# Kernel optimization log

Measured on AMD Instinct MI355X. Metric: run time of the kernel, lower is better.

Reference implementation:

```python
import jax, jax.numpy as jnp
import numpy as np

N = 65536   # query points
M = 65536   # support points
H = 32      # neighbors per query
IN = 64     # input feature dim
OUT = 64    # out_dim // 2
K = 15      # kernel points
EXTENT = 0.1 * 1.2 / 2.5  # radius * kp_extent / conv_radius = 0.048
BN_EPS = 1e-5


def setup_inputs() -> dict:
    key = jax.random.key(0)
    ks = jax.random.split(key, 8)
    x = jax.random.normal(ks[0], (M, IN), dtype=jnp.float32)
    q_pts = jax.random.uniform(ks[1], (N, 3), dtype=jnp.float32) * 0.1
    s_pts = jax.random.uniform(ks[2], (M, 3), dtype=jnp.float32) * 0.1
    neighb_inds = jax.random.randint(ks[3], (N, H), 0, M, dtype=jnp.int32)
    kernel_points = jax.random.normal(ks[4], (K, 3), dtype=jnp.float32) * (0.5 * EXTENT)
    weights = jax.random.normal(ks[5], (K, IN, OUT), dtype=jnp.float32) * 0.05
    gamma = jnp.ones((OUT,), dtype=jnp.float32)
    beta = jnp.zeros((OUT,), dtype=jnp.float32)
    return {"x": x, "q_pts": q_pts, "s_pts": s_pts, "neighb_inds": neighb_inds,
            "kernel_points": kernel_points, "weights": weights,
            "gamma": gamma, "beta": beta}


def reference(x, q_pts, s_pts, neighb_inds, kernel_points, weights, gamma, beta):
    # --- KPConv (rigid, linear influence, sum aggregation) ---
    # Shadow point/feature for out-of-range neighbor indices (KPConv convention).
    s_pad = jnp.concatenate([s_pts, jnp.full((1, 3), 1e6, s_pts.dtype)], axis=0)
    x_pad = jnp.concatenate([x, jnp.zeros((1, x.shape[1]), x.dtype)], axis=0)

    # Relative neighbor coordinates: [N, H, 3]
    neighbors = s_pad[neighb_inds] - q_pts[:, None, :]
    # Squared distance to each kernel point: [N, H, K]
    diffs = neighbors[:, :, None, :] - kernel_points[None, None, :, :]
    sq_dist = jnp.sum(diffs * diffs, axis=-1)
    # Linear kernel-point influence, clipped at 0: [N, H, K]
    all_weights = jnp.maximum(1.0 - jnp.sqrt(sq_dist) / EXTENT, 0.0)

    # Gather neighbor features: [N, H, IN]
    neighb_x = x_pad[neighb_inds]
    # Influence-weighted aggregation per kernel point: [N, K, IN]
    weighted = jnp.einsum('nhk,nhi->nki', all_weights, neighb_x)
    # Apply per-kernel-point weight matrices and sum over kernel points: [N, OUT]
    out = jnp.einsum('nki,kio->no', weighted, weights)

    # --- BatchNorm (training-mode statistics over points) ---
    mean = jnp.mean(out, axis=0)
    var = jnp.var(out, axis=0)
    out = (out - mean) / jnp.sqrt(var + BN_EPS) * gamma + beta

    # --- LeakyReLU(0.1) ---
    return jnp.where(out >= 0, out, 0.1 * out)
```

## Files before the change

kernel.cpp:

```cpp
#include <hip/hip_runtime.h>
#include <math.h>

#define NQ   65536
#define H    32
#define IN   64
#define OUTC 64
#define K    15
#define QB   16
#define S_XN 68
#define S_WT 36
#define AK   72
#define AROW 1076
#define INV_EXT (1.0f / 0.048f)

#define OFF_PSUM  131072
#define OFF_SCSH  (OFF_PSUM + 2097152)
#define OFF_XBF   (OFF_SCSH + 1024)
#define NEED_BF16 (OFF_XBF + (size_t)NQ * IN * 2)

typedef __attribute__((ext_vector_type(8))) short short8;
typedef __attribute__((ext_vector_type(4))) short short4v;
typedef __attribute__((ext_vector_type(4))) float float4v;

static __device__ __forceinline__ unsigned short f2bf(float f) {
    return (unsigned short)((__float_as_uint(f) + 0x8000u) >> 16);
}
static __device__ __forceinline__ unsigned pk2(float a, float b) {
    return (__float_as_uint(a) + 0x8000u) >> 16 |
           ((__float_as_uint(b) + 0x8000u) & 0xFFFF0000u);
}

__global__ __launch_bounds__(256) void prep_all(
    const float* __restrict__ W, const float* __restrict__ x,
    short* __restrict__ Bfrag, unsigned short* __restrict__ xbf, int do_x)
{
    const int b = blockIdx.x;
    if (b < 4096) {
        if (do_x) {
            const int t = b * 256 + threadIdx.x;
            const float4 v = ((const float4*)x)[t];
            uint2 p; p.x = pk2(v.x, v.y); p.y = pk2(v.z, v.w);
            ((uint2*)xbf)[t] = p;
        }
    } else {
        const int t2 = (b - 4096) * 256 + threadIdx.x;
        const int o  = t2 & 63;
        const int i  = (t2 >> 6) & 63;
        const int kq = t2 >> 12;
        const int t  = kq * 2 + (i >> 5);
        const int lane = ((i >> 3) & 3) * 16 + (o & 15);
        const int v  = o >> 4;
        const int j  = i & 7;
        Bfrag[((v * 30 + t) * 64 + lane) * 8 + j] = (short)f2bf(W[t2]);
    }
}

template<bool BFX>
__global__ __launch_bounds__(256, 4) void kpconv_mfma(
    const float* __restrict__ x, const unsigned short* __restrict__ xbf,
    const float* __restrict__ qp, const float* __restrict__ sp,
    const int* __restrict__ inds, const float* __restrict__ kp,
    const short* __restrict__ Bfrag, float* __restrict__ out_raw,
    float* __restrict__ psum)
{
    __shared__ __align__(16) short lds[17920];
    short* xn  = lds;
    short* wT  = lds + 8704;
    short* Awt = lds;

    const int tid  = threadIdx.x;
    const int lane = tid & 63;
    const int wv   = tid >> 6;
    const int quad = lane >> 4;
    const int ml   = lane & 15;
    const int q0   = blockIdx.x * QB;

    short4v xv[8];
    float4  xf[8];
    {
        const int ibase = (q0 + wv) * H;
#pragma unroll
        for (int j = 0; j < 8; ++j) {
            const int id = inds[ibase + j * 4 + quad];
            if (BFX) xv[j] = *(const short4v*)((const short*)xbf + id * IN + ml * 4);
            else     xf[j] = *(const float4*)(x + id * IN + ml * 4);
        }
    }

    for (int rep = 0; rep < 2; ++rep) {
        const int pair = tid + rep * 256;
        const int q = pair >> 5, h = pair & 31;
        const int n = q0 + q;
        const int id = inds[n * H + h];
        const float dx = sp[id * 3 + 0] - qp[n * 3 + 0];
        const float dy = sp[id * 3 + 1] - qp[n * 3 + 1];
        const float dz = sp[id * 3 + 2] - qp[n * 3 + 2];
#pragma unroll
        for (int k = 0; k < K; ++k) {
            const float ex = dx - kp[k * 3 + 0];
            const float ey = dy - kp[k * 3 + 1];
            const float ez = dz - kp[k * 3 + 2];
            const float sq = ex * ex + ey * ey + ez * ez;
            float wval = 1.0f - __builtin_amdgcn_sqrtf(sq) * INV_EXT;
            wval = wval > 0.0f ? wval : 0.0f;
            wT[(q * 16 + k) * S_WT + h] = (short)f2bf(wval);
        }
        wT[(q * 16 + K) * S_WT + h] = 0;
    }

    float4v frag[QB];
#pragma unroll
    for (int qg = 0; qg < QB; ++qg) frag[qg] = (float4v){0.f, 0.f, 0.f, 0.f};

    for (int b = 0; b < 4; ++b) {
#pragma unroll
        for (int j = 0; j < 8; ++j) {
            const int h = j * 4 + quad;
            if (BFX) {
                *(short4v*)&xn[(wv * H + h) * S_XN + ml * 4] = xv[j];
            } else {
                short4v p;
                p[0] = (short)f2bf(xf[j].x); p[1] = (short)f2bf(xf[j].y);
                p[2] = (short)f2bf(xf[j].z); p[3] = (short)f2bf(xf[j].w);
                *(short4v*)&xn[(wv * H + h) * S_XN + ml * 4] = p;
            }
        }
        __syncthreads();

        if (b < 3) {
            const int ibase = (q0 + 4 * (b + 1) + wv) * H;
#pragma unroll
            for (int j = 0; j < 8; ++j) {
                const int id = inds[ibase + j * 4 + quad];
                if (BFX) xv[j] = *(const short4v*)((const short*)xbf + id * IN + ml * 4);
                else     xf[j] = *(const float4*)(x + id * IN + ml * 4);
            }
        }

#pragma unroll
        for (int ql = 0; ql < 4; ++ql) {
            const int qg = 4 * b + ql;
            const int arow = (qg * 16 + ml) * S_WT + quad * 8;
            const short4v alo = *(const short4v*)&wT[arow];
            const short4v ahi = *(const short4v*)&wT[arow + 4];
            short8 a;
#pragma unroll
            for (int e = 0; e < 4; ++e) { a[e] = alo[e]; a[e + 4] = ahi[e]; }
            short8 bb;
#pragma unroll
            for (int j = 0; j < 8; ++j)
                bb[j] = xn[(ql * H + quad * 8 + j) * S_XN + wv * 16 + ml];
            frag[qg] = __builtin_amdgcn_mfma_f32_16x16x32_bf16(a, bb, frag[qg], 0, 0, 0);
        }
        __syncthreads();
    }

#pragma unroll
    for (int qg = 0; qg < QB; ++qg) {
#pragma unroll
        for (int r = 0; r < 4; ++r) {
            const int kq = quad * 4 + r;
            if (kq < K)
                Awt[qg * AROW + kq * AK + wv * 16 + ml] = (short)f2bf(frag[qg][r]);
        }
    }
    __syncthreads();

    float4v acc = (float4v){0.f, 0.f, 0.f, 0.f};
    const short* bptr = Bfrag + (wv * 30) * 512 + lane * 8;
#pragma unroll 2
    for (int t = 0; t < 30; ++t) {
        const int abase = ml * AROW + (t >> 1) * AK + (t & 1) * 32 + quad * 8;
        const short4v alo = *(const short4v*)&Awt[abase];
        const short4v ahi = *(const short4v*)&Awt[abase + 4];
        short8 a;
#pragma unroll
        for (int e = 0; e < 4; ++e) { a[e] = alo[e]; a[e + 4] = ahi[e]; }
        const short8 bb = *(const short8*)(bptr + t * 512);
        acc = __builtin_amdgcn_mfma_f32_16x16x32_bf16(a, bb, acc, 0, 0, 0);
    }

    float s = 0.f, s2 = 0.f;
#pragma unroll
    for (int r = 0; r < 4; ++r) {
        const float v = acc[r];
        out_raw[(q0 + quad * 4 + r) * OUTC + wv * 16 + ml] = v;
        s += v; s2 += v * v;
    }
    s  += __shfl_xor(s, 16, 64);  s  += __shfl_xor(s, 32, 64);
    s2 += __shfl_xor(s2, 16, 64); s2 += __shfl_xor(s2, 32, 64);
    if (quad == 0) {
        const int c = wv * 16 + ml;
        psum[c * 4096 + blockIdx.x]          = s;
        psum[262144 + c * 4096 + blockIdx.x] = s2;
    }
}

__global__ __launch_bounds__(256) void bn_stats(
    const float* __restrict__ psum, const float* __restrict__ gamma,
    const float* __restrict__ beta, float* __restrict__ sc_sh)
{
    const int c = blockIdx.x;
    const int t = threadIdx.x;
    float s = 0.f, q = 0.f;
#pragma unroll
    for (int i = 0; i < 16; ++i) {
        s += psum[c * 4096 + t + i * 256];
        q += psum[262144 + c * 4096 + t + i * 256];
    }
    __shared__ float rs[4], rq[4];
#pragma unroll
    for (int off = 32; off; off >>= 1) {
        s += __shfl_down(s, off, 64);
        q += __shfl_down(q, off, 64);
    }
    if ((t & 63) == 0) { rs[t >> 6] = s; rq[t >> 6] = q; }
    __syncthreads();
    if (t == 0) {
        s = rs[0] + rs[1] + rs[2] + rs[3];
        q = rq[0] + rq[1] + rq[2] + rq[3];
        const float mean = s * (1.0f / (float)NQ);
        const float var  = q * (1.0f / (float)NQ) - mean * mean;
        const float scale = gamma[c] / sqrtf(var + 1e-5f);
        sc_sh[c]      = scale;
        sc_sh[64 + c] = beta[c] - mean * scale;
    }
}

__global__ __launch_bounds__(256) void bn_apply(
    float* __restrict__ out, const float* __restrict__ sc_sh)
{
    __shared__ float sc[64];
    __shared__ float sh[64];
    if (threadIdx.x < 64) {
        sc[threadIdx.x] = sc_sh[threadIdx.x];
        sh[threadIdx.x] = sc_sh[64 + threadIdx.x];
    }
    __syncthreads();
    const int idx = blockIdx.x * 256 + threadIdx.x;
#pragma unroll
    for (int it = 0; it < 4; ++it) {
        const int e = idx + it * 262144;
        float4 v = ((const float4*)out)[e];
        const int cg = (e & 15) * 4;
        float4 r;
        r.x = v.x * sc[cg + 0] + sh[cg + 0];
        r.y = v.y * sc[cg + 1] + sh[cg + 1];
        r.z = v.z * sc[cg + 2] + sh[cg + 2];
        r.w = v.w * sc[cg + 3] + sh[cg + 3];
        r.x = r.x >= 0.0f ? r.x : 0.1f * r.x;
        r.y = r.y >= 0.0f ? r.y : 0.1f * r.y;
        r.z = r.z >= 0.0f ? r.z : 0.1f * r.z;
        r.w = r.w >= 0.0f ? r.w : 0.1f * r.w;
        ((float4*)out)[e] = r;
    }
}

extern "C" void kernel_launch(void* const* d_in, const int* in_sizes, int n_in,
                              void* d_out, int out_size, void* d_ws, size_t ws_size,
                              hipStream_t stream)
{
    (void)in_sizes; (void)n_in; (void)out_size;
    const float* x     = (const float*)d_in[0];
    const float* qp    = (const float*)d_in[1];
    const float* sp    = (const float*)d_in[2];
    const int*   inds  = (const int*)d_in[3];
    const float* kp    = (const float*)d_in[4];
    const float* W     = (const float*)d_in[5];
    const float* gamma = (const float*)d_in[6];
    const float* beta  = (const float*)d_in[7];
    float* out = (float*)d_out;

    short*          Bfrag = (short*)d_ws;
    float*          psum  = (float*)((char*)d_ws + OFF_PSUM);
    float*          sc_sh = (float*)((char*)d_ws + OFF_SCSH);
    unsigned short* xbf   = (unsigned short*)((char*)d_ws + OFF_XBF);

    const int use_bf = (ws_size >= NEED_BF16) ? 1 : 0;

    prep_all<<<4336, 256, 0, stream>>>(W, x, Bfrag, xbf, use_bf);
    if (use_bf)
        kpconv_mfma<true><<<NQ / QB, 256, 0, stream>>>(x, xbf, qp, sp, inds, kp, Bfrag, out, psum);
    else
        kpconv_mfma<false><<<NQ / QB, 256, 0, stream>>>(x, xbf, qp, sp, inds, kp, Bfrag, out, psum);
    bn_stats<<<64, 256, 0, stream>>>(psum, gamma, beta, sc_sh);
    bn_apply<<<1024, 256, 0, stream>>>(out, sc_sh);
}
```

Before: 155.6 us.

## Give each wave its own queries to drop block barriers in aggregation

Work is redistributed so each wave owns four queries. It computes their kernel-point influence weights, gathers their neighbor features into a private LDS slice, and runs the first MFMA stage over all four 16-column output slices of its own queries. Because waves no longer share LDS data during this stage, the per-batch __syncthreads pairs are removed and a single barrier remains before the results are written into the aliased Awt region. In exchange, each wave prefetches neighbor rows only one query ahead, and the weight-computation and MFMA work is split differently across waves.

```diff
diff --git a/kernel.cpp b/kernel.cpp
--- a/kernel.cpp
+++ b/kernel.cpp
@@ -75,10 +75,12 @@
     const int ml   = lane & 15;
     const int q0   = blockIdx.x * QB;
 
+    short* xn_own = xn + wv * (H * S_XN);
+
     short4v xv[8];
     float4  xf[8];
     {
-        const int ibase = (q0 + wv) * H;
+        const int ibase = (q0 + wv * 4) * H;
 #pragma unroll
         for (int j = 0; j < 8; ++j) {
             const int id = inds[ibase + j * 4 + quad];
@@ -88,9 +90,10 @@
     }
 
     for (int rep = 0; rep < 2; ++rep) {
-        const int pair = tid + rep * 256;
-        const int q = pair >> 5, h = pair & 31;
-        const int n = q0 + q;
+        const int p = lane + rep * 64;
+        const int qi = p >> 5, h = p & 31;
+        const int qg = wv * 4 + qi;
+        const int n = q0 + qg;
         const int id = inds[n * H + h];
         const float dx = sp[id * 3 + 0] - qp[n * 3 + 0];
         const float dy = sp[id * 3 + 1] - qp[n * 3 + 1];
@@ -103,32 +106,35 @@
             const float sq = ex * ex + ey * ey + ez * ez;
             float wval = 1.0f - __builtin_amdgcn_sqrtf(sq) * INV_EXT;
             wval = wval > 0.0f ? wval : 0.0f;
-            wT[(q * 16 + k) * S_WT + h] = (short)f2bf(wval);
-        }
-        wT[(q * 16 + K) * S_WT + h] = 0;
-    }
-
-    float4v frag[QB];
-#pragma unroll
-    for (int qg = 0; qg < QB; ++qg) frag[qg] = (float4v){0.f, 0.f, 0.f, 0.f};
-
-    for (int b = 0; b < 4; ++b) {
+            wT[(qg * 16 + k) * S_WT + h] = (short)f2bf(wval);
+        }
+        wT[(qg * 16 + K) * S_WT + h] = 0;
+    }
+
+    float4v frag[4][4];
+#pragma unroll
+    for (int qi = 0; qi < 4; ++qi)
+#pragma unroll
+        for (int v = 0; v < 4; ++v) frag[qi][v] = (float4v){0.f, 0.f, 0.f, 0.f};
+
+    for (int qi = 0; qi < 4; ++qi) {
+        const int qg = wv * 4 + qi;
+
 #pragma unroll
         for (int j = 0; j < 8; ++j) {
             const int h = j * 4 + quad;
             if (BFX) {
-                *(short4v*)&xn[(wv * H + h) * S_XN + ml * 4] = xv[j];
+                *(short4v*)&xn_own[h * S_XN + ml * 4] = xv[j];
             } else {
                 short4v p;
                 p[0] = (short)f2bf(xf[j].x); p[1] = (short)f2bf(xf[j].y);
                 p[2] = (short)f2bf(xf[j].z); p[3] = (short)f2bf(xf[j].w);
-                *(short4v*)&xn[(wv * H + h) * S_XN + ml * 4] = p;
+                *(short4v*)&xn_own[h * S_XN + ml * 4] = p;
             }
         }
-        __syncthreads();
-
-        if (b < 3) {
-            const int ibase = (q0 + 4 * (b + 1) + wv) * H;
+
+        if (qi < 3) {
+            const int ibase = (q0 + qg + 1) * H;
 #pragma unroll
             for (int j = 0; j < 8; ++j) {
                 const int id = inds[ibase + j * 4 + quad];
@@ -137,31 +143,36 @@
             }
         }
 
-#pragma unroll
-        for (int ql = 0; ql < 4; ++ql) {
-            const int qg = 4 * b + ql;
-            const int arow = (qg * 16 + ml) * S_WT + quad * 8;
-            const short4v alo = *(const short4v*)&wT[arow];
-            const short4v ahi = *(const short4v*)&wT[arow + 4];
-            short8 a;
-#pragma unroll
-            for (int e = 0; e < 4; ++e) { a[e] = alo[e]; a[e + 4] = ahi[e]; }
+        const int arow = (qg * 16 + ml) * S_WT + quad * 8;
+        const short4v alo = *(const short4v*)&wT[arow];
+        const short4v ahi = *(const short4v*)&wT[arow + 4];
+        short8 a;
+#pragma unroll
+        for (int e = 0; e < 4; ++e) { a[e] = alo[e]; a[e + 4] = ahi[e]; }
+
+#pragma unroll
+        for (int v = 0; v < 4; ++v) {
             short8 bb;
 #pragma unroll
             for (int j = 0; j < 8; ++j)
-                bb[j] = xn[(ql * H + quad * 8 + j) * S_XN + wv * 16 + ml];
-            frag[qg] = __builtin_amdgcn_mfma_f32_16x16x32_bf16(a, bb, frag[qg], 0, 0, 0);
-        }
-        __syncthreads();
-    }
-
-#pragma unroll
-    for (int qg = 0; qg < QB; ++qg) {
-#pragma unroll
-        for (int r = 0; r < 4; ++r) {
-            const int kq = quad * 4 + r;
-            if (kq < K)
-                Awt[qg * AROW + kq * AK + wv * 16 + ml] = (short)f2bf(frag[qg][r]);
+                bb[j] = xn_own[(quad * 8 + j) * S_XN + v * 16 + ml];
+            frag[qi][v] = __builtin_amdgcn_mfma_f32_16x16x32_bf16(a, bb, frag[qi][v], 0, 0, 0);
+        }
+    }
+
+    __syncthreads();
+
+#pragma unroll
+    for (int qi = 0; qi < 4; ++qi) {
+        const int qg = wv * 4 + qi;
+#pragma unroll
+        for (int v = 0; v < 4; ++v) {
+#pragma unroll
+            for (int r = 0; r < 4; ++r) {
+                const int kq = quad * 4 + r;
+                if (kq < K)
+                    Awt[qg * AROW + kq * AK + v * 16 + ml] = (short)f2bf(frag[qi][v][r]);
+            }
         }
     }
     __syncthreads();
```

New measurement: 152.7 us. About the same (-1.9%).
